# Kernel optimization log

Measured on AMD Instinct MI355X. Metric: run time of the kernel, lower is better.

The kernel has to match this reference:

```python
import jax, jax.numpy as jnp
import numpy as np

THETA = 10.0
TOP_K = 12
EPS = 1e-8  # torch F.cosine_similarity eps


def setup_inputs() -> dict:
    key = jax.random.key(0)
    h = jax.random.normal(key, (8192, 512), dtype=jnp.float32)
    return {"h": h}


def reference(h):
    # cosine similarity: normalize with clamped norm like torch (eps=1e-8)
    norm = jnp.linalg.norm(h, axis=-1, keepdims=True)
    hn = h / jnp.maximum(norm, EPS)
    # Sim[i, j] = cos(h[i], h[j]); [N, N]
    Sim = jnp.einsum('id,jd->ij', hn, hn)
    # top-k neighbors per row
    sim_topk, idx_topk = jax.lax.top_k(Sim, TOP_K)          # [N, k]
    beta = jax.nn.softmax(THETA * sim_topk, axis=-1)        # [N, k]
    h_topk = h[idx_topk]                                    # [N, k, d]
    # dropout is identity in eval mode
    h_sim = jnp.einsum('nk,nkd->nd', beta, h_topk)          # [N, d]
    return h_sim
```

## Files before the change

### kernel.cpp

```cpp
#include <hip/hip_runtime.h>
#include <hip/hip_bf16.h>

#define N 8192
#define D 512
#define K_TOP 12
#define THETA 10.0f
#define EPS 1e-8f
#define TAU 0.10f
#define CAPL 6
#define CAPG 192
#define NPAIR 2080
#define NBLK 1024

typedef float f32x16 __attribute__((ext_vector_type(16)));

__device__ __forceinline__ unsigned int bf16_bits_rne(float v) {
    unsigned int u = __float_as_uint(v);
    u += 0x7FFFu + ((u >> 16) & 1u);
    return u >> 16;
}

__device__ __forceinline__ void load16(const unsigned char* g, unsigned char* l) {
    __builtin_amdgcn_global_load_lds(
        (const __attribute__((address_space(1))) unsigned int*)g,
        (__attribute__((address_space(3))) unsigned int*)l, 16, 0, 0);
}

__device__ __forceinline__ void decode_pair(int p, int& it, int& jt) {
    int j = (int)((sqrtf(8.0f * (float)p + 1.0f) - 1.0f) * 0.5f);
    while ((j + 1) * (j + 2) / 2 <= p) ++j;
    while (j * (j + 1) / 2 > p) --j;
    jt = j;
    it = p - j * (j + 1) / 2;
}

__global__ __launch_bounds__(256) void norm_kernel(const float* __restrict__ h,
                                                   unsigned char* __restrict__ hq,
                                                   float* __restrict__ norms,
                                                   int* __restrict__ gcnt,
                                                   int* __restrict__ gflag) {
    int row = blockIdx.x * 4 + (threadIdx.x >> 6);
    int lane = threadIdx.x & 63;
    const float4* hr4 = (const float4*)(h + (size_t)row * D);
    float4 p0 = hr4[lane], p1 = hr4[64 + lane];
    float ss = p0.x * p0.x + p0.y * p0.y + p0.z * p0.z + p0.w * p0.w +
               p1.x * p1.x + p1.y * p1.y + p1.z * p1.z + p1.w * p1.w;
#pragma unroll
    for (int off = 32; off > 0; off >>= 1) ss += __shfl_xor(ss, off, 64);
    float nrm = fmaxf(sqrtf(ss), EPS);
    float inv = 1.0f / nrm;
    if (lane == 0) { gcnt[row] = 0; gflag[row] = 0; norms[row] = nrm; }
    unsigned int w0 = __builtin_amdgcn_cvt_pk_fp8_f32(p0.x * inv, p0.y * inv, 0, false);
    w0 = __builtin_amdgcn_cvt_pk_fp8_f32(p0.z * inv, p0.w * inv, w0, true);
    unsigned int w1 = __builtin_amdgcn_cvt_pk_fp8_f32(p1.x * inv, p1.y * inv, 0, false);
    w1 = __builtin_amdgcn_cvt_pk_fp8_f32(p1.z * inv, p1.w * inv, w1, true);
    unsigned int* q32 = (unsigned int*)(hq + (size_t)row * D);
    q32[lane] = w0;
    q32[64 + lane] = w1;
}

__global__ __launch_bounds__(256, 4) void simfp8_kernel(
        const unsigned char* __restrict__ hq,
        unsigned int* __restrict__ gcand,
        int* __restrict__ gcnt,
        int* __restrict__ gflag) {
    __shared__ unsigned char tiles[2][2][128 * 64];
    __shared__ int cnt[256];
    __shared__ unsigned int lbuf[256][CAPL];

    const int b = blockIdx.x;
    const int t = threadIdx.x;
    const int wave = t >> 6, lane = t & 63;
    const int wr = (wave >> 1) * 64, wc = (wave & 1) * 64;
    const int lm32 = lane & 31, lg2 = lane >> 5;
    const int rk = (lm32 >> 2) & 3;

    const int srow = t >> 2;
    const int sq = (t & 3) ^ ((t >> 4) & 3);

    cnt[t] = 0;

    auto issue = [&](int ii0, int jj0, int r_) {
        int sel = r_ & 1;
        const unsigned char* gA = hq + (size_t)(ii0 + srow) * D + r_ * 64 + sq * 16;
        const unsigned char* gB = hq + (size_t)(jj0 + srow) * D + r_ * 64 + sq * 16;
        unsigned char* lA = &tiles[sel][0][t * 16];
        unsigned char* lB = &tiles[sel][1][t * 16];
#pragma unroll
        for (int e = 0; e < 2; e++) {
            load16(gA + (size_t)(e * 64) * D, lA + e * 4096);
            load16(gB + (size_t)(e * 64) * D, lB + e * 4096);
        }
    };

    const int nloc = (b + 2048 < NPAIR) ? 3 : 2;

    int it, jt;
    decode_pair(b, it, jt);
    int ci0 = it * 128, cj0 = jt * 128;
    bool cdiag = (it == jt);
    issue(ci0, cj0, 0);

    f32x16 acc[2][2];
#pragma unroll
    for (int x = 0; x < 2; x++)
#pragma unroll
        for (int y = 0; y < 2; y++)
#pragma unroll
            for (int q = 0; q < 16; q++) acc[x][y][q] = 0.f;

    for (int qp = 0; qp < nloc; qp++) {
        int ni0 = 0, nj0 = 0;
        bool ndiag = false;
        if (qp + 1 < nloc) {
            int i2, j2;
            decode_pair(b + (qp + 1) * NBLK, i2, j2);
            ni0 = i2 * 128; nj0 = j2 * 128; ndiag = (i2 == j2);
        }

        for (int r = 0; r < 8; r++) {
            const int sel = r & 1;

            __builtin_amdgcn_s_barrier();
            if (r < 7) {
                issue(ci0, cj0, r + 1);
                asm volatile("s_waitcnt vmcnt(4)" ::: "memory");
            } else if (qp + 1 < nloc) {
                issue(ni0, nj0, 0);
                asm volatile("s_waitcnt vmcnt(4)" ::: "memory");
            } else {
                asm volatile("s_waitcnt vmcnt(0)" ::: "memory");
            }
            __builtin_amdgcn_s_barrier();

#pragma unroll
            for (int kk = 0; kk < 4; kk++) {
                const int kb = ((kk ^ rk) << 4) + lg2 * 8;
                long long af[2], bfr[2];
#pragma unroll
                for (int x = 0; x < 2; x++)
                    af[x] = *(const long long*)&tiles[sel][0][(wr + x * 32 + lm32) * 64 + kb];
#pragma unroll
                for (int y = 0; y < 2; y++)
                    bfr[y] = *(const long long*)&tiles[sel][1][(wc + y * 32 + lm32) * 64 + kb];
#pragma unroll
                for (int x = 0; x < 2; x++)
#pragma unroll
                    for (int y = 0; y < 2; y++)
                        acc[x][y] = __builtin_amdgcn_mfma_f32_32x32x16_fp8_fp8(
                            af[x], bfr[y], acc[x][y], 0, 0, 0);
            }
        }

#pragma unroll
        for (int x = 0; x < 2; x++)
#pragma unroll
            for (int y = 0; y < 2; y++) {
                int lcol = wc + y * 32 + lm32;
                int gcol = cj0 + lcol;
#pragma unroll
                for (int q = 0; q < 16; q++) {
                    int rr = wr + x * 32 + (q & 3) + 8 * (q >> 2) + 4 * lg2;
                    int gi = ci0 + rr;
                    float v = acc[x][y][q];
                    acc[x][y][q] = 0.f;
                    if (gi == gcol) v = 1.0f;
                    if (v > TAU) {
                        unsigned int vb = bf16_bits_rne(v) << 16;
                        int idx = atomicAdd(&cnt[rr], 1);
                        if (idx < CAPL) lbuf[rr][idx] = vb | (unsigned int)gcol;
                        else {
                            int pg = atomicAdd(&gcnt[gi], 1);
                            if (pg < CAPG) gcand[(size_t)gi * CAPG + pg] = vb | (unsigned int)gcol;
                            else gflag[gi] = 1;
                        }
                        if (!cdiag) {
                            int idx2 = atomicAdd(&cnt[128 + lcol], 1);
                            if (idx2 < CAPL) lbuf[128 + lcol][idx2] = vb | (unsigned int)gi;
                            else {
                                int pg = atomicAdd(&gcnt[gcol], 1);
                                if (pg < CAPG) gcand[(size_t)gcol * CAPG + pg] = vb | (unsigned int)gi;
                                else gflag[gcol] = 1;
                            }
                        }
                    }
                }
            }

        __syncthreads();
        {
            int grow = (t < 128) ? (ci0 + t) : (cj0 + t - 128);
            int c = cnt[t];
            int s = c < CAPL ? c : CAPL;
            if (s > 0) {
                int base = atomicAdd(&gcnt[grow], s);
                unsigned int* dst = gcand + (size_t)grow * CAPG;
                for (int k = 0; k < s; k++) {
                    int pp = base + k;
                    if (pp < CAPG) dst[pp] = lbuf[t][k];
                    else gflag[grow] = 1;
                }
            }
            cnt[t] = 0;
        }

        ci0 = ni0; cj0 = nj0; cdiag = ndiag;
    }
}

__global__ __launch_bounds__(256) void gather_kernel(const float* __restrict__ h,
                                                     const unsigned char* __restrict__ hq,
                                                     const float* __restrict__ norms,
                                                     const unsigned int* __restrict__ gcand,
                                                     const int* __restrict__ gcnt,
                                                     const int* __restrict__ gflag,
                                                     float* __restrict__ out) {
    int row = blockIdx.x * 4 + (threadIdx.x >> 6);
    int lane = threadIdx.x & 63;

    const float4* hr4 = (const float4*)(h + (size_t)row * D);
    float4 s0 = hr4[lane], s1 = hr4[64 + lane];

    int c = gcnt[row];

    float selv[K_TOP];
    int selj[K_TOP];

    if (c >= K_TOP && c <= CAPG && gflag[row] == 0) {
        const unsigned int* cr = gcand + (size_t)row * CAPG;
        unsigned int e[3];
#pragma unroll
        for (int q = 0; q < 3; q++) {
            int idx = lane + 64 * q;
            e[q] = (idx < c) ? cr[idx] : 0u;
        }
#pragma unroll
        for (int k = 0; k < K_TOP; k++) {
            unsigned int m = e[0];
            if (e[1] > m) m = e[1];
            if (e[2] > m) m = e[2];
#pragma unroll
            for (int off = 32; off > 0; off >>= 1) {
                unsigned int om = __shfl_xor(m, off, 64);
                if (om > m) m = om;
            }
            selv[k] = __uint_as_float(m & 0xFFFF0000u);
            selj[k] = (int)(m & 0x1FFFu);
#pragma unroll
            for (int q = 0; q < 3; q++)
                if (e[q] == m) e[q] = 0u;
        }
    } else {
        float vals[K_TOP];
        int idxs[K_TOP];
#pragma unroll
        for (int q = 0; q < K_TOP; q++) { vals[q] = -3e38f; idxs[q] = 0; }
        float minv = -3e38f;
        int minp = 0;
        const unsigned int* rp = (const unsigned int*)(hq + (size_t)row * D);
        for (int col = lane; col < N; col += 64) {
            const unsigned int* cp = (const unsigned int*)(hq + (size_t)col * D);
            float s = 0.f;
            for (int k4 = 0; k4 < D / 4; k4++) {
                unsigned int ra = rp[k4], ca = cp[k4];
                s += __builtin_amdgcn_cvt_f32_fp8(ra, 0) * __builtin_amdgcn_cvt_f32_fp8(ca, 0);
                s += __builtin_amdgcn_cvt_f32_fp8(ra, 1) * __builtin_amdgcn_cvt_f32_fp8(ca, 1);
                s += __builtin_amdgcn_cvt_f32_fp8(ra, 2) * __builtin_amdgcn_cvt_f32_fp8(ca, 2);
                s += __builtin_amdgcn_cvt_f32_fp8(ra, 3) * __builtin_amdgcn_cvt_f32_fp8(ca, 3);
            }
            if (col == row) s = 1.0f;
            if (s > minv) {
                vals[minp] = s; idxs[minp] = col;
                minv = vals[0]; minp = 0;
#pragma unroll
                for (int q = 1; q < K_TOP; q++)
                    if (vals[q] < minv) { minv = vals[q]; minp = q; }
            }
        }
        for (int k = 0; k < K_TOP; k++) {
            float bv = vals[0]; int bp = 0;
#pragma unroll
            for (int q = 1; q < K_TOP; q++)
                if (vals[q] > bv) { bv = vals[q]; bp = q; }
            float v = bv; int j = idxs[bp]; int src = lane;
#pragma unroll
            for (int off = 32; off > 0; off >>= 1) {
                float ov = __shfl_xor(v, off, 64);
                int oj = __shfl_xor(j, off, 64);
                int os = __shfl_xor(src, off, 64);
                if (ov > v || (ov == v && os < src)) { v = ov; j = oj; src = os; }
            }
            selv[k] = __uint_as_float((unsigned int)(bf16_bits_rne(v) << 16));
            selj[k] = j;
            if (lane == src) vals[bp] = -3e38f;
        }
    }

    unsigned int na[K_TOP], nb[K_TOP];
    float wn[K_TOP];
#pragma unroll
    for (int q = 0; q < K_TOP; q++) {
        const unsigned int* r32 = (const unsigned int*)(hq + (size_t)selj[q] * D);
        na[q] = r32[lane];
        nb[q] = r32[64 + lane];
        wn[q] = norms[selj[q]];
    }

    float mx = selv[0];
    float beta[K_TOP];
    float sum = 0.f;
#pragma unroll
    for (int q = 0; q < K_TOP; q++) { beta[q] = __expf(THETA * (selv[q] - mx)); sum += beta[q]; }
    float rs = 1.0f / sum;

    float acc[8];
#pragma unroll
    for (int ee = 0; ee < 8; ee++) acc[ee] = 0.f;
#pragma unroll
    for (int q = 0; q < K_TOP; q++) {
        float w = beta[q] * rs;
        if (selj[q] == row) {
            acc[0] += w * s0.x; acc[1] += w * s0.y; acc[2] += w * s0.z; acc[3] += w * s0.w;
            acc[4] += w * s1.x; acc[5] += w * s1.y; acc[6] += w * s1.z; acc[7] += w * s1.w;
        } else {
            float wj = w * wn[q];
            acc[0] += wj * __builtin_amdgcn_cvt_f32_fp8(na[q], 0);
            acc[1] += wj * __builtin_amdgcn_cvt_f32_fp8(na[q], 1);
            acc[2] += wj * __builtin_amdgcn_cvt_f32_fp8(na[q], 2);
            acc[3] += wj * __builtin_amdgcn_cvt_f32_fp8(na[q], 3);
            acc[4] += wj * __builtin_amdgcn_cvt_f32_fp8(nb[q], 0);
            acc[5] += wj * __builtin_amdgcn_cvt_f32_fp8(nb[q], 1);
            acc[6] += wj * __builtin_amdgcn_cvt_f32_fp8(nb[q], 2);
            acc[7] += wj * __builtin_amdgcn_cvt_f32_fp8(nb[q], 3);
        }
    }
    float4* o4 = (float4*)(out + (size_t)row * D);
    o4[lane] = make_float4(acc[0], acc[1], acc[2], acc[3]);
    o4[64 + lane] = make_float4(acc[4], acc[5], acc[6], acc[7]);
}

extern "C" void kernel_launch(void* const* d_in, const int* in_sizes, int n_in,
                              void* d_out, int out_size, void* d_ws, size_t ws_size,
                              hipStream_t stream) {
    const float* h = (const float*)d_in[0];
    float* out = (float*)d_out;

    char* ws = (char*)d_ws;
    unsigned char* hq = (unsigned char*)ws;
    size_t off = (size_t)N * D;
    float* norms = (float*)(ws + off);
    int* gcnt = (int*)(ws + off + (size_t)N * 4);
    int* gflag = (int*)(ws + off + (size_t)N * 8);
    unsigned int* gcand = (unsigned int*)(ws + off + (size_t)N * 12);

    norm_kernel<<<N / 4, 256, 0, stream>>>(h, hq, norms, gcnt, gflag);
    simfp8_kernel<<<NBLK, 256, 0, stream>>>(hq, gcand, gcnt, gflag);
    gather_kernel<<<N / 4, 256, 0, stream>>>(h, hq, norms, gcand, gcnt, gflag, out);
}
```

Baseline: 132.5 us.

## Switch to single-buffered 128-wide K tiles with MFMA priority boost

Tiles are now staged as 128-byte K chunks in a single LDS buffer, which halves the number of barrier-separated stages per pair tile. The double-buffered prefetch of the next chunk and next tile pair is removed, and each stage waits for all loads to finish. s_setprio is raised around the MFMA loop. The change cuts loop and barrier overhead but gives up overlap between global loads and compute, relying on other resident blocks to hide latency.

```diff
diff --git a/kernel.cpp b/kernel.cpp
--- a/kernel.cpp
+++ b/kernel.cpp
@@ -64,7 +64,7 @@
         unsigned int* __restrict__ gcand,
         int* __restrict__ gcnt,
         int* __restrict__ gflag) {
-    __shared__ unsigned char tiles[2][2][128 * 64];
+    __shared__ unsigned char tiles[2][128 * 128];
     __shared__ int cnt[256];
     __shared__ unsigned int lbuf[256][CAPL];
 
@@ -73,34 +73,27 @@
     const int wave = t >> 6, lane = t & 63;
     const int wr = (wave >> 1) * 64, wc = (wave & 1) * 64;
     const int lm32 = lane & 31, lg2 = lane >> 5;
-    const int rk = (lm32 >> 2) & 3;
-
-    const int srow = t >> 2;
-    const int sq = (t & 3) ^ ((t >> 4) & 3);
+    const int rk = lm32 & 7;
+
+    const int srow = t >> 3;
+    const int sq = (t & 7) ^ ((t >> 3) & 7);
 
     cnt[t] = 0;
 
-    auto issue = [&](int ii0, int jj0, int r_) {
-        int sel = r_ & 1;
-        const unsigned char* gA = hq + (size_t)(ii0 + srow) * D + r_ * 64 + sq * 16;
-        const unsigned char* gB = hq + (size_t)(jj0 + srow) * D + r_ * 64 + sq * 16;
-        unsigned char* lA = &tiles[sel][0][t * 16];
-        unsigned char* lB = &tiles[sel][1][t * 16];
-#pragma unroll
-        for (int e = 0; e < 2; e++) {
-            load16(gA + (size_t)(e * 64) * D, lA + e * 4096);
-            load16(gB + (size_t)(e * 64) * D, lB + e * 4096);
+    auto stage = [&](int ii0, int jj0, int r_) {
+        const unsigned char* gA = hq + (size_t)(ii0 + srow) * D + r_ * 128 + sq * 16;
+        const unsigned char* gB = hq + (size_t)(jj0 + srow) * D + r_ * 128 + sq * 16;
+        unsigned char* lA = &tiles[0][t * 16];
+        unsigned char* lB = &tiles[1][t * 16];
+#pragma unroll
+        for (int e = 0; e < 4; e++) {
+            load16(gA + (size_t)(e * 32) * D, lA + e * 4096);
+            load16(gB + (size_t)(e * 32) * D, lB + e * 4096);
         }
     };
 
     const int nloc = (b + 2048 < NPAIR) ? 3 : 2;
 
-    int it, jt;
-    decode_pair(b, it, jt);
-    int ci0 = it * 128, cj0 = jt * 128;
-    bool cdiag = (it == jt);
-    issue(ci0, cj0, 0);
-
     f32x16 acc[2][2];
 #pragma unroll
     for (int x = 0; x < 2; x++)
@@ -110,39 +103,28 @@
             for (int q = 0; q < 16; q++) acc[x][y][q] = 0.f;
 
     for (int qp = 0; qp < nloc; qp++) {
-        int ni0 = 0, nj0 = 0;
-        bool ndiag = false;
-        if (qp + 1 < nloc) {
-            int i2, j2;
-            decode_pair(b + (qp + 1) * NBLK, i2, j2);
-            ni0 = i2 * 128; nj0 = j2 * 128; ndiag = (i2 == j2);
-        }
-
-        for (int r = 0; r < 8; r++) {
-            const int sel = r & 1;
-
+        int it, jt;
+        decode_pair(b + qp * NBLK, it, jt);
+        const int ci0 = it * 128, cj0 = jt * 128;
+        const bool cdiag = (it == jt);
+
+        for (int r = 0; r < 4; r++) {
             __builtin_amdgcn_s_barrier();
-            if (r < 7) {
-                issue(ci0, cj0, r + 1);
-                asm volatile("s_waitcnt vmcnt(4)" ::: "memory");
-            } else if (qp + 1 < nloc) {
-                issue(ni0, nj0, 0);
-                asm volatile("s_waitcnt vmcnt(4)" ::: "memory");
-            } else {
-                asm volatile("s_waitcnt vmcnt(0)" ::: "memory");
-            }
+            stage(ci0, cj0, r);
+            asm volatile("s_waitcnt vmcnt(0)" ::: "memory");
             __builtin_amdgcn_s_barrier();
 
-#pragma unroll
-            for (int kk = 0; kk < 4; kk++) {
+            __builtin_amdgcn_s_setprio(1);
+#pragma unroll
+            for (int kk = 0; kk < 8; kk++) {
                 const int kb = ((kk ^ rk) << 4) + lg2 * 8;
                 long long af[2], bfr[2];
 #pragma unroll
                 for (int x = 0; x < 2; x++)
-                    af[x] = *(const long long*)&tiles[sel][0][(wr + x * 32 + lm32) * 64 + kb];
+                    af[x] = *(const long long*)&tiles[0][(wr + x * 32 + lm32) * 128 + kb];
 #pragma unroll
                 for (int y = 0; y < 2; y++)
-                    bfr[y] = *(const long long*)&tiles[sel][1][(wc + y * 32 + lm32) * 64 + kb];
+                    bfr[y] = *(const long long*)&tiles[1][(wc + y * 32 + lm32) * 128 + kb];
 #pragma unroll
                 for (int x = 0; x < 2; x++)
 #pragma unroll
@@ -150,6 +132,7 @@
                         acc[x][y] = __builtin_amdgcn_mfma_f32_32x32x16_fp8_fp8(
                             af[x], bfr[y], acc[x][y], 0, 0, 0);
             }
+            __builtin_amdgcn_s_setprio(0);
         }
 
 #pragma unroll
@@ -203,8 +186,6 @@
             }
             cnt[t] = 0;
         }
-
-        ci0 = ni0; cj0 = nj0; cdiag = ndiag;
     }
 }
 
```

After: 135.1 us. About the same (+1.9%).

## Replace static tile-pair assignment with atomic work stealing in similarity kernel

Applied to the files above, without the earlier changes.

The similarity kernel used to give each block a fixed set of 2 or 3 upper-triangular tile pairs, which leaves some blocks running one extra pair at the tail. Blocks now take their next tile pair from a global atomic counter, reset by the norm kernel, so faster blocks pick up remaining work. This adds one atomic and a shared-memory broadcast per tile, and the next tile's prefetch now waits on the atomic result. The counter lives in workspace after the candidate buffer.

```diff
diff --git a/kernel.cpp b/kernel.cpp
--- a/kernel.cpp
+++ b/kernel.cpp
@@ -38,9 +38,11 @@
                                                    unsigned char* __restrict__ hq,
                                                    float* __restrict__ norms,
                                                    int* __restrict__ gcnt,
-                                                   int* __restrict__ gflag) {
+                                                   int* __restrict__ gflag,
+                                                   int* __restrict__ steal) {
     int row = blockIdx.x * 4 + (threadIdx.x >> 6);
     int lane = threadIdx.x & 63;
+    if (blockIdx.x == 0 && threadIdx.x == 0) steal[0] = NBLK;
     const float4* hr4 = (const float4*)(h + (size_t)row * D);
     float4 p0 = hr4[lane], p1 = hr4[64 + lane];
     float ss = p0.x * p0.x + p0.y * p0.y + p0.z * p0.z + p0.w * p0.w +
@@ -63,10 +65,12 @@
         const unsigned char* __restrict__ hq,
         unsigned int* __restrict__ gcand,
         int* __restrict__ gcnt,
-        int* __restrict__ gflag) {
+        int* __restrict__ gflag,
+        int* __restrict__ steal) {
     __shared__ unsigned char tiles[2][2][128 * 64];
     __shared__ int cnt[256];
     __shared__ unsigned int lbuf[256][CAPL];
+    __shared__ int nextp_sh;
 
     const int b = blockIdx.x;
     const int t = threadIdx.x;
@@ -93,12 +97,10 @@
         }
     };
 
-    const int nloc = (b + 2048 < NPAIR) ? 3 : 2;
-
-    int it, jt;
-    decode_pair(b, it, jt);
-    int ci0 = it * 128, cj0 = jt * 128;
-    bool cdiag = (it == jt);
+    int cit, cjt;
+    decode_pair(b, cit, cjt);
+    int ci0 = cit * 128, cj0 = cjt * 128;
+    bool cdiag = (cit == cjt);
     issue(ci0, cj0, 0);
 
     f32x16 acc[2][2];
@@ -109,14 +111,11 @@
 #pragma unroll
             for (int q = 0; q < 16; q++) acc[x][y][q] = 0.f;
 
-    for (int qp = 0; qp < nloc; qp++) {
-        int ni0 = 0, nj0 = 0;
+    for (;;) {
+        if (t == 0) nextp_sh = atomicAdd(steal, 1);
+
+        int np = NPAIR, ni0 = 0, nj0 = 0;
         bool ndiag = false;
-        if (qp + 1 < nloc) {
-            int i2, j2;
-            decode_pair(b + (qp + 1) * NBLK, i2, j2);
-            ni0 = i2 * 128; nj0 = j2 * 128; ndiag = (i2 == j2);
-        }
 
         for (int r = 0; r < 8; r++) {
             const int sel = r & 1;
@@ -125,11 +124,17 @@
             if (r < 7) {
                 issue(ci0, cj0, r + 1);
                 asm volatile("s_waitcnt vmcnt(4)" ::: "memory");
-            } else if (qp + 1 < nloc) {
-                issue(ni0, nj0, 0);
-                asm volatile("s_waitcnt vmcnt(4)" ::: "memory");
             } else {
-                asm volatile("s_waitcnt vmcnt(0)" ::: "memory");
+                np = nextp_sh;
+                if (np < NPAIR) {
+                    int nit, njt;
+                    decode_pair(np, nit, njt);
+                    ni0 = nit * 128; nj0 = njt * 128; ndiag = (nit == njt);
+                    issue(ni0, nj0, 0);
+                    asm volatile("s_waitcnt vmcnt(4)" ::: "memory");
+                } else {
+                    asm volatile("s_waitcnt vmcnt(0)" ::: "memory");
+                }
             }
             __builtin_amdgcn_s_barrier();
 
@@ -204,7 +209,10 @@
             cnt[t] = 0;
         }
 
-        ci0 = ni0; cj0 = nj0; cdiag = ndiag;
+        if (np >= NPAIR) break;
+        ci0 = ni0; cj0 = nj0;
+        cdiag = ndiag;
+        decode_pair(np, cit, cjt);
     }
 }
 
@@ -352,8 +360,9 @@
     int* gcnt = (int*)(ws + off + (size_t)N * 4);
     int* gflag = (int*)(ws + off + (size_t)N * 8);
     unsigned int* gcand = (unsigned int*)(ws + off + (size_t)N * 12);
-
-    norm_kernel<<<N / 4, 256, 0, stream>>>(h, hq, norms, gcnt, gflag);
-    simfp8_kernel<<<NBLK, 256, 0, stream>>>(hq, gcand, gcnt, gflag);
+    int* steal = (int*)(ws + off + (size_t)N * 12 + (size_t)N * CAPG * 4);
+
+    norm_kernel<<<N / 4, 256, 0, stream>>>(h, hq, norms, gcnt, gflag, steal);
+    simfp8_kernel<<<NBLK, 256, 0, stream>>>(hq, gcand, gcnt, gflag, steal);
     gather_kernel<<<N / 4, 256, 0, stream>>>(h, hq, norms, gcand, gcnt, gflag, out);
 }
```

New measurement: 144.4 us. 1.09x slower.

## Rebalance tile pairs so every block does two tiles plus split leftover strips

Applied to the files above, without the earlier changes.

Previously 2080 triangular tile pairs were spread over 1024 blocks, so 32 blocks ran a third 128x128 tile and set the tail of the schedule. Now every block runs exactly two full tiles, and the 32 leftover pairs (row tiles 32..63 paired with tile 63) are split into 64 half-width 128x64 strips handled by the first 64 blocks. The goal is to shorten the critical path by evening out per-block work. The cost is extra code paths: a separate strip load routine and a second MFMA, threshold and candidate-flush epilogue.

```diff
diff --git a/kernel.cpp b/kernel.cpp
--- a/kernel.cpp
+++ b/kernel.cpp
@@ -78,6 +78,10 @@
     const int srow = t >> 2;
     const int sq = (t & 3) ^ ((t >> 4) & 3);
 
+    const int i0s = (32 + (b >> 1)) * 128;
+    const int j0s = 63 * 128 + (b & 1) * 64;
+    const bool sdiag = ((b >> 1) == 31);
+
     cnt[t] = 0;
 
     auto issue = [&](int ii0, int jj0, int r_) {
@@ -93,12 +97,28 @@
         }
     };
 
-    const int nloc = (b + 2048 < NPAIR) ? 3 : 2;
-
-    int it, jt;
-    decode_pair(b, it, jt);
-    int ci0 = it * 128, cj0 = jt * 128;
-    bool cdiag = (it == jt);
+    auto issue_strip = [&](int r_) {
+        int sel = r_ & 1;
+        const unsigned char* gA = hq + (size_t)(i0s + srow) * D + r_ * 64 + sq * 16;
+        const unsigned char* gB = hq + (size_t)(j0s + srow) * D + r_ * 64 + sq * 16;
+        unsigned char* lA = &tiles[sel][0][t * 16];
+#pragma unroll
+        for (int e = 0; e < 2; e++)
+            load16(gA + (size_t)(e * 64) * D, lA + e * 4096);
+        load16(gB, &tiles[sel][1][t * 16]);
+    };
+
+    int cit, cjt;
+    decode_pair(b, cit, cjt);
+    int ci0 = cit * 128, cj0 = cjt * 128;
+    bool cdiag = (cit == cjt);
+    int ni0 = 0, nj0 = 0;
+    bool ndiag = false;
+    {
+        int nit, njt;
+        decode_pair(b + NBLK, nit, njt);
+        ni0 = nit * 128; nj0 = njt * 128; ndiag = (nit == njt);
+    }
     issue(ci0, cj0, 0);
 
     f32x16 acc[2][2];
@@ -109,15 +129,7 @@
 #pragma unroll
             for (int q = 0; q < 16; q++) acc[x][y][q] = 0.f;
 
-    for (int qp = 0; qp < nloc; qp++) {
-        int ni0 = 0, nj0 = 0;
-        bool ndiag = false;
-        if (qp + 1 < nloc) {
-            int i2, j2;
-            decode_pair(b + (qp + 1) * NBLK, i2, j2);
-            ni0 = i2 * 128; nj0 = j2 * 128; ndiag = (i2 == j2);
-        }
-
+    for (int qp = 0; qp < 2; qp++) {
         for (int r = 0; r < 8; r++) {
             const int sel = r & 1;
 
@@ -125,9 +137,12 @@
             if (r < 7) {
                 issue(ci0, cj0, r + 1);
                 asm volatile("s_waitcnt vmcnt(4)" ::: "memory");
-            } else if (qp + 1 < nloc) {
+            } else if (qp == 0) {
                 issue(ni0, nj0, 0);
                 asm volatile("s_waitcnt vmcnt(4)" ::: "memory");
+            } else if (b < 64) {
+                issue_strip(0);
+                asm volatile("s_waitcnt vmcnt(3)" ::: "memory");
             } else {
                 asm volatile("s_waitcnt vmcnt(0)" ::: "memory");
             }
@@ -206,6 +221,93 @@
 
         ci0 = ni0; cj0 = nj0; cdiag = ndiag;
     }
+
+    if (b >= 64) return;
+
+    {
+        const int wr2 = wave * 32;
+        f32x16 sacc[2];
+#pragma unroll
+        for (int y = 0; y < 2; y++)
+#pragma unroll
+            for (int q = 0; q < 16; q++) sacc[y][q] = 0.f;
+
+        for (int r = 0; r < 8; r++) {
+            const int sel = r & 1;
+
+            __builtin_amdgcn_s_barrier();
+            if (r < 7) {
+                issue_strip(r + 1);
+                asm volatile("s_waitcnt vmcnt(3)" ::: "memory");
+            } else {
+                asm volatile("s_waitcnt vmcnt(0)" ::: "memory");
+            }
+            __builtin_amdgcn_s_barrier();
+
+#pragma unroll
+            for (int kk = 0; kk < 4; kk++) {
+                const int kb = ((kk ^ rk) << 4) + lg2 * 8;
+                long long af =
+                    *(const long long*)&tiles[sel][0][(wr2 + lm32) * 64 + kb];
+                long long bfr[2];
+#pragma unroll
+                for (int y = 0; y < 2; y++)
+                    bfr[y] = *(const long long*)&tiles[sel][1][(y * 32 + lm32) * 64 + kb];
+#pragma unroll
+                for (int y = 0; y < 2; y++)
+                    sacc[y] = __builtin_amdgcn_mfma_f32_32x32x16_fp8_fp8(
+                        af, bfr[y], sacc[y], 0, 0, 0);
+            }
+        }
+
+#pragma unroll
+        for (int y = 0; y < 2; y++) {
+            int lcol = y * 32 + lm32;
+            int gcol = j0s + lcol;
+#pragma unroll
+            for (int q = 0; q < 16; q++) {
+                int rr = wr2 + (q & 3) + 8 * (q >> 2) + 4 * lg2;
+                int gi = i0s + rr;
+                float v = sacc[y][q];
+                if (gi == gcol) v = 1.0f;
+                if (v > TAU) {
+                    unsigned int vb = bf16_bits_rne(v) << 16;
+                    int idx = atomicAdd(&cnt[rr], 1);
+                    if (idx < CAPL) lbuf[rr][idx] = vb | (unsigned int)gcol;
+                    else {
+                        int pg = atomicAdd(&gcnt[gi], 1);
+                        if (pg < CAPG) gcand[(size_t)gi * CAPG + pg] = vb | (unsigned int)gcol;
+                        else gflag[gi] = 1;
+                    }
+                    if (!sdiag) {
+                        int idx2 = atomicAdd(&cnt[128 + lcol], 1);
+                        if (idx2 < CAPL) lbuf[128 + lcol][idx2] = vb | (unsigned int)gi;
+                        else {
+                            int pg = atomicAdd(&gcnt[gcol], 1);
+                            if (pg < CAPG) gcand[(size_t)gcol * CAPG + pg] = vb | (unsigned int)gi;
+                            else gflag[gcol] = 1;
+                        }
+                    }
+                }
+            }
+        }
+
+        __syncthreads();
+        if (t < 192) {
+            int grow = (t < 128) ? (i0s + t) : (j0s + t - 128);
+            int c = cnt[t];
+            int s = c < CAPL ? c : CAPL;
+            if (s > 0) {
+                int base = atomicAdd(&gcnt[grow], s);
+                unsigned int* dst = gcand + (size_t)grow * CAPG;
+                for (int k = 0; k < s; k++) {
+                    int pp = base + k;
+                    if (pp < CAPG) dst[pp] = lbuf[t][k];
+                    else gflag[grow] = 1;
+                }
+            }
+        }
+    }
 }
 
 __global__ __launch_bounds__(256) void gather_kernel(const float* __restrict__ h,
```

New measurement: 130.8 us. No clear change (-1.3%).
